# Optimization experiments

Measured on AMD Instinct MI355X. Metric: run time of the kernel, lower is better.

## Reference

```python
import jax, jax.numpy as jnp
import numpy as np

N = 100000   # nodes per graph
E = 1200000  # edges per graph
V = 50000    # vocab
EMB = 100    # embedding size
H = 64       # hidden size
B = 4096     # selected nodes (batch)
TIMESTEPS = 3  # per layer, layer_timesteps=[3,3]


def setup_inputs() -> dict:
    key = jax.random.key(0)
    ks = jax.random.split(key, 32)
    s = 0.05
    d = {}
    d['emb_ind_0'] = jax.random.randint(ks[0], (N,), 0, V)
    d['emb_ind_1'] = jax.random.randint(ks[1], (N,), 0, V)
    d['adj_0'] = jax.random.randint(ks[2], (E, 2), 0, N)
    d['adj_1'] = jax.random.randint(ks[3], (E, 2), 0, N)
    d['prop_ind_0'] = jax.random.randint(ks[4], (B,), 0, N)
    d['prop_ind_1'] = jax.random.randint(ks[5], (B,), 0, N)
    d['labels'] = jax.random.randint(ks[6], (B,), 0, 2)
    # embedding table (padding_idx=0 row zeroed)
    emb = jax.random.normal(ks[7], (V, EMB), jnp.float32) * s
    d['emb_table'] = emb.at[0].set(0.0)
    # emb_proj Linear(EMB, H)
    d['Wp'] = jax.random.normal(ks[8], (EMB, H), jnp.float32) * s
    d['bp'] = jnp.zeros((H,), jnp.float32)
    # GGNN: 2 layers, 1 edge type each; edge message Linear + GRUCell
    for l in range(2):
        o = 9 + 6 * l
        d[f'Wm{l}'] = jax.random.normal(ks[o + 0], (H, H), jnp.float32) * s
        d[f'bm{l}'] = jnp.zeros((H,), jnp.float32)
        d[f'Wih{l}'] = jax.random.normal(ks[o + 2], (H, 3 * H), jnp.float32) * s
        d[f'Whh{l}'] = jax.random.normal(ks[o + 3], (H, 3 * H), jnp.float32) * s
        d[f'bih{l}'] = jnp.zeros((3 * H,), jnp.float32)
        d[f'bhh{l}'] = jnp.zeros((3 * H,), jnp.float32)
    # classifier MLP: Linear(2H, H) -> ReLU -> Linear(H, 1) (dropout = identity in eval)
    d['W1'] = jax.random.normal(ks[22], (2 * H, H), jnp.float32) * s
    d['b1'] = jnp.zeros((H,), jnp.float32)
    d['W2'] = jax.random.normal(ks[23], (H, 1), jnp.float32) * s
    d['b2'] = jnp.zeros((1,), jnp.float32)
    return d


def gru_cell(x, h, Wih, Whh, bih, bhh):
    gi = x @ Wih + bih                       # [N, 3H]
    gh = h @ Whh + bhh
    ir, iz, ig = jnp.split(gi, 3, axis=-1)   # torch GRUCell gate order: r, z, n
    hr, hz, hg = jnp.split(gh, 3, axis=-1)
    r = jax.nn.sigmoid(ir + hr)
    z = jax.nn.sigmoid(iz + hz)
    n = jnp.tanh(ig + r * hg)
    return (1.0 - z) * n + z * h


def ggnn(h, edges, layer_params):
    src, tgt = edges[:, 0], edges[:, 1]
    n_nodes = h.shape[0]
    for (Wm, bm, Wih, Whh, bih, bhh) in layer_params:
        for _ in range(TIMESTEPS):
            msg = h[src] @ Wm + bm                                  # gather + edge transform [E, H]
            agg = jax.ops.segment_sum(msg, tgt, num_segments=n_nodes)  # scatter-add [N, H]
            h = gru_cell(agg, h, Wih, Whh, bih, bhh)
    return h


def reference(emb_ind_0, emb_ind_1, adj_0, adj_1, prop_ind_0, prop_ind_1, labels,
              emb_table, Wp, bp,
              Wm0, bm0, Wih0, Whh0, bih0, bhh0,
              Wm1, bm1, Wih1, Whh1, bih1, bhh1,
              W1, b1, W2, b2):
    layer_params = [(Wm0, bm0, Wih0, Whh0, bih0, bhh0),
                    (Wm1, bm1, Wih1, Whh1, bih1, bhh1)]
    ge_list = []
    for emb_ind, adj, prop_ind in ((emb_ind_0, adj_0, prop_ind_0),
                                   (emb_ind_1, adj_1, prop_ind_1)):
        ge = emb_table[emb_ind] @ Wp + bp        # embed + project [N, H]
        ge = ggnn(ge, adj, layer_params)
        ge_list.append(ge[prop_ind])             # index_select [B, H]
    ge = jnp.concatenate(ge_list, axis=-1)       # [B, 2H]
    hidden = jax.nn.relu(ge @ W1 + b1)
    z = hidden @ W2 + b2                         # [B, 1]
    probs = jax.nn.sigmoid(z)                    # torch code returns sigmoid as 'logits'
    y = labels.astype(z.dtype)
    zf = z[:, 0]
    # BCELoss(sigmoid(z), y), stably: log p = log_sigmoid(z), log(1-p) = log_sigmoid(-z)
    loss = -jnp.mean(y * jax.nn.log_sigmoid(zf) + (1.0 - y) * jax.nn.log_sigmoid(-zf))
    return (probs, loss)
```

## Files before the change

### kernel.cpp

```cpp
#include <hip/hip_runtime.h>
#include <math.h>

#define NN 100000
#define NN2 200000
#define NE 1200000
#define EMBD 100
#define HD 64
#define BT 4096
#define SCAN_B 196

typedef __attribute__((ext_vector_type(8))) short short8;
typedef __attribute__((ext_vector_type(4))) float f32x4;
typedef __attribute__((ext_vector_type(2))) float f32x2;

__device__ __forceinline__ float sig1(float x) { return 1.f / (1.f + __expf(-x)); }
__device__ __forceinline__ float tanh1(float x) {
    x = fminf(fmaxf(x, -15.f), 15.f);
    float e = __expf(2.f * x);
    return (e - 1.f) / (e + 1.f);
}
__device__ __forceinline__ unsigned short f2b(float f) {
    unsigned u = __float_as_uint(f);
    u += 0x7fffu + ((u >> 16) & 1u);
    return (unsigned short)(u >> 16);
}
__device__ __forceinline__ unsigned short hi16(float f) {
    return (unsigned short)(__float_as_uint(f) >> 16);
}
__device__ __forceinline__ unsigned packb(float lo, float hi) {
    return (unsigned)f2b(lo) | ((unsigned)f2b(hi) << 16);
}
__device__ __forceinline__ unsigned pk8(float a, float b, float c, float d) {
    int w = 0;
    w = __builtin_amdgcn_cvt_pk_fp8_f32(a, b, w, false);
    w = __builtin_amdgcn_cvt_pk_fp8_f32(c, d, w, true);
    return (unsigned)w;
}
__device__ __forceinline__ short8 f8frag(uint2 u) {
    const f32x2 a0 = __builtin_amdgcn_cvt_pk_f32_fp8(u.x, false);
    const f32x2 a1 = __builtin_amdgcn_cvt_pk_f32_fp8(u.x, true);
    const f32x2 a2 = __builtin_amdgcn_cvt_pk_f32_fp8(u.y, false);
    const f32x2 a3 = __builtin_amdgcn_cvt_pk_f32_fp8(u.y, true);
    short8 r;
    r[0] = (short)hi16(a0.x); r[1] = (short)hi16(a0.y);
    r[2] = (short)hi16(a1.x); r[3] = (short)hi16(a1.y);
    r[4] = (short)hi16(a2.x); r[5] = (short)hi16(a2.y);
    r[6] = (short)hi16(a3.x); r[7] = (short)hi16(a3.y);
    return r;
}

__global__ __launch_bounds__(256) void fusew_kernel(
    const float* __restrict__ Wm0, const float* __restrict__ Wih0, const float* __restrict__ bm0,
    const float* __restrict__ Wm1, const float* __restrict__ Wih1, const float* __restrict__ bm1,
    float* __restrict__ Wf, float* __restrict__ bf) {
    extern __shared__ float lds[];
    float* wm_s = lds;
    float* wih_s = lds + 4096;
    const int l = blockIdx.x >> 3, slice = blockIdx.x & 7;
    const float* Wm = l ? Wm1 : Wm0;
    const float* Wih = l ? Wih1 : Wih0;
    const float* bm = l ? bm1 : bm0;
    for (int i = threadIdx.x; i < 4096; i += 256) wm_s[i] = Wm[i];
    for (int i = threadIdx.x; i < 12288; i += 256) wih_s[i] = Wih[i];
    __syncthreads();
    float* Wfl = Wf + l * 12288;
    float* bfl = bf + l * 192;
    const int o0 = slice * 1536;
    for (int o = o0 + threadIdx.x; o < o0 + 1536; o += 256) {
        int r = o / 192, c = o % 192;
        float s = 0.f;
        for (int k = 0; k < 64; ++k) s = fmaf(wm_s[r * 64 + k], wih_s[k * 192 + c], s);
        Wfl[o] = s;
    }
    const int c0 = slice * 24;
    for (int c = c0 + threadIdx.x; c < c0 + 24; c += 256) {
        float s = 0.f;
        for (int k = 0; k < 64; ++k) s = fmaf(bm[k], wih_s[k * 192 + c], s);
        bfl[c] = s;
    }
}

__global__ __launch_bounds__(64) void wpack_kernel(
    const float* __restrict__ Wf, const float* __restrict__ Whh0, const float* __restrict__ Whh1,
    unsigned short* __restrict__ Wpk) {
    const int b = blockIdx.x;
    const int l = b >> 6, frag = b & 63;
    const int nt = frag >> 2, kk = frag & 3;
    const int lane = threadIdx.x;
    const int n = nt * 16 + (lane & 15);
    const int g = n >> 6, j = n & 63;
    const int k0 = kk * 32 + (lane >> 4) * 8;
    const float* wf = Wf + l * 12288;
    const float* whh = l ? Whh1 : Whh0;
    unsigned short o[8];
#pragma unroll
    for (int jj = 0; jj < 8; ++jj) {
        const int k = k0 + jj;
        float v = 0.f;
        if (k < 64) {
            const int kp = (k & 3) * 16 + (k >> 2);
            if (g == 0) v = wf[kp * 192 + j];
            else if (g == 1) v = wf[kp * 192 + 64 + j];
            else if (g == 2) v = wf[kp * 192 + 128 + j];
        } else {
            const int kp = ((k - 64) & 3) * 16 + ((k - 64) >> 2);
            if (g == 0) v = whh[kp * 192 + j];
            else if (g == 1) v = whh[kp * 192 + 64 + j];
            else if (g == 3) v = whh[kp * 192 + 128 + j];
        }
        o[jj] = f2b(v);
    }
    *(uint4*)(Wpk + ((size_t)(l * 64 + frag) * 64 + lane) * 8) = *(const uint4*)o;
}

__global__ __launch_bounds__(256) void embed_kernel(
    const int* __restrict__ ind0, const int* __restrict__ ind1, const float* __restrict__ emb,
    const float* __restrict__ Wp, const float* __restrict__ bp,
    unsigned char* __restrict__ hb8) {
    __shared__ float et[4][EMBD][4];
    const int w = threadIdx.x >> 6;
    const int l = threadIdx.x & 63;
    const int nodeBase = blockIdx.x * 16 + w * 4;
    for (int f = l; f < 100; f += 64) {
        const int n = f / 25, c = f % 25;
        const int gn = nodeBase + n;
        const int idx = (gn < NN) ? ind0[gn] : ind1[gn - NN];
        const float4 v = *(const float4*)(emb + (size_t)idx * EMBD + c * 4);
        et[w][c * 4 + 0][n] = v.x;
        et[w][c * 4 + 1][n] = v.y;
        et[w][c * 4 + 2][n] = v.z;
        et[w][c * 4 + 3][n] = v.w;
    }
    __syncthreads();
    float acc[4];
    acc[0] = bp[l]; acc[1] = acc[0]; acc[2] = acc[0]; acc[3] = acc[0];
#pragma unroll 5
    for (int k = 0; k < EMBD; ++k) {
        const float wv = Wp[k * 64 + l];
        const float4 ev = *(const float4*)&et[w][k][0];
        acc[0] = fmaf(ev.x, wv, acc[0]);
        acc[1] = fmaf(ev.y, wv, acc[1]);
        acc[2] = fmaf(ev.z, wv, acc[2]);
        acc[3] = fmaf(ev.w, wv, acc[3]);
    }
#pragma unroll
    for (int n = 0; n < 4; ++n) {
        const float v0 = __shfl(acc[n], l & 15);
        const float v1 = __shfl(acc[n], (l & 15) + 16);
        const float v2 = __shfl(acc[n], (l & 15) + 32);
        const float v3 = __shfl(acc[n], (l & 15) + 48);
        if (l < 16) ((unsigned*)(hb8 + (size_t)(nodeBase + n) * 64))[l] = pk8(v0, v1, v2, v3);
    }
}

__global__ __launch_bounds__(256) void hist_kernel(
    const int* __restrict__ adj0, const int* __restrict__ adj1, int* __restrict__ rowptr,
    int* __restrict__ rank) {
    const int e = blockIdx.x * 256 + threadIdx.x;
    const int tgt = (e < NE) ? adj0[2 * e + 1] : adj1[2 * (e - NE) + 1] + NN;
    rank[e] = atomicAdd(&rowptr[tgt], 1);
}

__global__ __launch_bounds__(256) void scan1_kernel(const int* __restrict__ rowptr, int* __restrict__ bsum) {
    __shared__ int red[256];
    const int t = threadIdx.x, b = blockIdx.x;
    const int base = b * 1024;
    int s = 0;
    for (int i = t; i < 1024; i += 256) {
        const int idx = base + i;
        s += (idx < NN2) ? rowptr[idx] : 0;
    }
    red[t] = s;
    __syncthreads();
    for (int off = 128; off > 0; off >>= 1) {
        if (t < off) red[t] += red[t + off];
        __syncthreads();
    }
    if (t == 0) bsum[b] = red[0];
}

__global__ __launch_bounds__(256) void scan2_kernel(int* __restrict__ bsum) {
    __shared__ int s[256];
    const int t = threadIdx.x;
    const int v = (t < SCAN_B) ? bsum[t] : 0;
    s[t] = v;
    __syncthreads();
    for (int off = 1; off < 256; off <<= 1) {
        const int x = (t >= off) ? s[t - off] : 0;
        __syncthreads();
        s[t] += x;
        __syncthreads();
    }
    if (t < SCAN_B) bsum[t] = s[t] - v;
}

__global__ __launch_bounds__(256) void scan3_kernel(int* __restrict__ rowptr, const int* __restrict__ bsum,
                                                    float* __restrict__ deg) {
    __shared__ int red[256];
    const int t = threadIdx.x, b = blockIdx.x;
    const int i0 = b * 1024 + t * 4;
    int v[4];
#pragma unroll
    for (int j = 0; j < 4; ++j) v[j] = (i0 + j < NN2) ? rowptr[i0 + j] : 0;
    const int ts = v[0] + v[1] + v[2] + v[3];
    red[t] = ts;
    __syncthreads();
    for (int off = 1; off < 256; off <<= 1) {
        const int x = (t >= off) ? red[t - off] : 0;
        __syncthreads();
        red[t] += x;
        __syncthreads();
    }
    int pre = bsum[b] + red[t] - ts;
#pragma unroll
    for (int j = 0; j < 4; ++j) {
        if (i0 + j < NN2) {
            rowptr[i0 + j] = pre;
            deg[i0 + j] = (float)v[j];
            pre += v[j];
        }
    }
}

__global__ __launch_bounds__(256) void fill_kernel(
    const int* __restrict__ adj0, const int* __restrict__ adj1,
    const int* __restrict__ rowptr, const int* __restrict__ rank, int* __restrict__ csr) {
    const int e = blockIdx.x * 256 + threadIdx.x;
    int2 st;
    int off;
    if (e < NE) {
        st = ((const int2*)adj0)[e];
        off = 0;
    } else {
        st = ((const int2*)adj1)[e - NE];
        off = NN;
    }
    const int tgt = st.y + off;
    csr[rowptr[tgt] + rank[e]] = st.x + off;
}

__global__ __launch_bounds__(256) void agg_kernel(
    const int* __restrict__ rowptr, const int* __restrict__ csr,
    const unsigned char* __restrict__ hb8, unsigned short* __restrict__ aggb) {
    const int t = threadIdx.x;
    const int node = blockIdx.x * 64 + (t >> 2);
    const int c = t & 3;
    const int start = rowptr[node];
    const int end = (node + 1 < NN2) ? rowptr[node + 1] : 2 * NE;
    float acc[16];
#pragma unroll
    for (int j = 0; j < 16; ++j) acc[j] = 0.f;
    int e = start;
    for (; e + 3 < end; e += 4) {
        int s[4];
        uint4 u[4];
#pragma unroll
        for (int q = 0; q < 4; ++q) s[q] = csr[e + q];
#pragma unroll
        for (int q = 0; q < 4; ++q) u[q] = *(const uint4*)(hb8 + (size_t)s[q] * 64 + c * 16);
#pragma unroll
        for (int q = 0; q < 4; ++q) {
            const f32x2 a0 = __builtin_amdgcn_cvt_pk_f32_fp8(u[q].x, false);
            const f32x2 a1 = __builtin_amdgcn_cvt_pk_f32_fp8(u[q].x, true);
            const f32x2 a2 = __builtin_amdgcn_cvt_pk_f32_fp8(u[q].y, false);
            const f32x2 a3 = __builtin_amdgcn_cvt_pk_f32_fp8(u[q].y, true);
            const f32x2 a4 = __builtin_amdgcn_cvt_pk_f32_fp8(u[q].z, false);
            const f32x2 a5 = __builtin_amdgcn_cvt_pk_f32_fp8(u[q].z, true);
            const f32x2 a6 = __builtin_amdgcn_cvt_pk_f32_fp8(u[q].w, false);
            const f32x2 a7 = __builtin_amdgcn_cvt_pk_f32_fp8(u[q].w, true);
            acc[0] += a0.x; acc[1] += a0.y; acc[2] += a1.x; acc[3] += a1.y;
            acc[4] += a2.x; acc[5] += a2.y; acc[6] += a3.x; acc[7] += a3.y;
            acc[8] += a4.x; acc[9] += a4.y; acc[10] += a5.x; acc[11] += a5.y;
            acc[12] += a6.x; acc[13] += a6.y; acc[14] += a7.x; acc[15] += a7.y;
        }
    }
    for (; e < end; ++e) {
        const uint4 u = *(const uint4*)(hb8 + (size_t)csr[e] * 64 + c * 16);
        const f32x2 a0 = __builtin_amdgcn_cvt_pk_f32_fp8(u.x, false);
        const f32x2 a1 = __builtin_amdgcn_cvt_pk_f32_fp8(u.x, true);
        const f32x2 a2 = __builtin_amdgcn_cvt_pk_f32_fp8(u.y, false);
        const f32x2 a3 = __builtin_amdgcn_cvt_pk_f32_fp8(u.y, true);
        const f32x2 a4 = __builtin_amdgcn_cvt_pk_f32_fp8(u.z, false);
        const f32x2 a5 = __builtin_amdgcn_cvt_pk_f32_fp8(u.z, true);
        const f32x2 a6 = __builtin_amdgcn_cvt_pk_f32_fp8(u.w, false);
        const f32x2 a7 = __builtin_amdgcn_cvt_pk_f32_fp8(u.w, true);
        acc[0] += a0.x; acc[1] += a0.y; acc[2] += a1.x; acc[3] += a1.y;
        acc[4] += a2.x; acc[5] += a2.y; acc[6] += a3.x; acc[7] += a3.y;
        acc[8] += a4.x; acc[9] += a4.y; acc[10] += a5.x; acc[11] += a5.y;
        acc[12] += a6.x; acc[13] += a6.y; acc[14] += a7.x; acc[15] += a7.y;
    }
    uint4 o0, o1;
    o0.x = packb(acc[0], acc[1]);
    o0.y = packb(acc[2], acc[3]);
    o0.z = packb(acc[4], acc[5]);
    o0.w = packb(acc[6], acc[7]);
    o1.x = packb(acc[8], acc[9]);
    o1.y = packb(acc[10], acc[11]);
    o1.z = packb(acc[12], acc[13]);
    o1.w = packb(acc[14], acc[15]);
    *(uint4*)(aggb + node * 64 + c * 16) = o0;
    *(uint4*)(aggb + node * 64 + c * 16 + 8) = o1;
}

__global__ __launch_bounds__(256) void aggx_kernel(
    const int* __restrict__ prop0, const int* __restrict__ prop1,
    const int* __restrict__ rowptr, const int* __restrict__ csr,
    const unsigned char* __restrict__ hb8, unsigned short* __restrict__ aggX) {
    const int t = threadIdx.x;
    const int p = blockIdx.x * 64 + (t >> 2);
    const int c = t & 3;
    const int node = (p < BT) ? prop0[p] : NN + prop1[p - BT];
    const int start = rowptr[node];
    const int end = (node + 1 < NN2) ? rowptr[node + 1] : 2 * NE;
    float acc[16];
#pragma unroll
    for (int j = 0; j < 16; ++j) acc[j] = 0.f;
    for (int e = start; e < end; ++e) {
        const uint4 u = *(const uint4*)(hb8 + (size_t)csr[e] * 64 + c * 16);
        const f32x2 a0 = __builtin_amdgcn_cvt_pk_f32_fp8(u.x, false);
        const f32x2 a1 = __builtin_amdgcn_cvt_pk_f32_fp8(u.x, true);
        const f32x2 a2 = __builtin_amdgcn_cvt_pk_f32_fp8(u.y, false);
        const f32x2 a3 = __builtin_amdgcn_cvt_pk_f32_fp8(u.y, true);
        const f32x2 a4 = __builtin_amdgcn_cvt_pk_f32_fp8(u.z, false);
        const f32x2 a5 = __builtin_amdgcn_cvt_pk_f32_fp8(u.z, true);
        const f32x2 a6 = __builtin_amdgcn_cvt_pk_f32_fp8(u.w, false);
        const f32x2 a7 = __builtin_amdgcn_cvt_pk_f32_fp8(u.w, true);
        acc[0] += a0.x; acc[1] += a0.y; acc[2] += a1.x; acc[3] += a1.y;
        acc[4] += a2.x; acc[5] += a2.y; acc[6] += a3.x; acc[7] += a3.y;
        acc[8] += a4.x; acc[9] += a4.y; acc[10] += a5.x; acc[11] += a5.y;
        acc[12] += a6.x; acc[13] += a6.y; acc[14] += a7.x; acc[15] += a7.y;
    }
    uint4 o0, o1;
    o0.x = packb(acc[0], acc[1]);
    o0.y = packb(acc[2], acc[3]);
    o0.z = packb(acc[4], acc[5]);
    o0.w = packb(acc[6], acc[7]);
    o1.x = packb(acc[8], acc[9]);
    o1.y = packb(acc[10], acc[11]);
    o1.z = packb(acc[12], acc[13]);
    o1.w = packb(acc[14], acc[15]);
    *(uint4*)(aggX + p * 64 + c * 16) = o0;
    *(uint4*)(aggX + p * 64 + c * 16 + 8) = o1;
}

__global__ __launch_bounds__(256) void gru_mfma_kernel(
    unsigned char* __restrict__ hb8, const unsigned short* __restrict__ aggb,
    const float* __restrict__ deg, const unsigned short* __restrict__ Wpk,
    const float* __restrict__ bf, const float* __restrict__ bih, const float* __restrict__ bhh) {
    extern __shared__ unsigned short ldsW[];
    {
        const uint4* src = (const uint4*)Wpk;
        uint4* dst = (uint4*)ldsW;
        for (int i = threadIdx.x; i < 4096; i += 256) dst[i] = src[i];
    }
    __syncthreads();
    const int lane = threadIdx.x & 63;
    const int j0 = lane & 15, quad = lane >> 4;
    const int q8 = quad * 8;
    float cr[4], cz[4], cig[4], chg[4], vbfr[4], vbfz[4], vbfg[4];
#pragma unroll
    for (int c4 = 0; c4 < 4; ++c4) {
        const int col = c4 * 16 + j0;
        cr[c4] = bih[col] + bhh[col];
        cz[c4] = bih[64 + col] + bhh[64 + col];
        cig[c4] = bih[128 + col];
        chg[c4] = bhh[128 + col];
        vbfr[c4] = bf[col];
        vbfz[c4] = bf[64 + col];
        vbfg[c4] = bf[128 + col];
    }
    const short8* ldsW8 = (const short8*)ldsW;
    const int gw = blockIdx.x * 4 + (threadIdx.x >> 6);
    const int nw = gridDim.x * 4;

    auto epilogue = [&](const f32x4(&acc)[16], int nb) {
#pragma unroll
        for (int reg = 0; reg < 4; ++reg) {
            const int node = nb + reg;
            const float dg = deg[node];
            const unsigned hu = *(const unsigned*)(hb8 + (size_t)node * 64 + j0 * 4);
            const f32x2 h01 = __builtin_amdgcn_cvt_pk_f32_fp8(hu, false);
            const f32x2 h23 = __builtin_amdgcn_cvt_pk_f32_fp8(hu, true);
            const float holdf[4] = {h01.x, h01.y, h23.x, h23.y};
            float hn[4];
#pragma unroll
            for (int c4 = 0; c4 < 4; ++c4) {
                const float rv = sig1(acc[c4][reg] + cr[c4] + dg * vbfr[c4]);
                const float zv = sig1(acc[4 + c4][reg] + cz[c4] + dg * vbfz[c4]);
                const float gi = acc[8 + c4][reg] + cig[c4] + dg * vbfg[c4];
                const float gh = acc[12 + c4][reg] + chg[c4];
                const float nv = tanh1(fmaf(rv, gh, gi));
                hn[c4] = (1.f - zv) * nv + zv * holdf[c4];
            }
            ((unsigned*)(hb8 + (size_t)node * 64))[j0] = pk8(hn[0], hn[1], hn[2], hn[3]);
        }
    };

    for (int t = gw; t < NN2 / 32; t += nw) {
        const int mbase = t * 32;
        const int node0 = mbase + j0, node1 = node0 + 16;
        short8 a[4], b[4];
        a[0] = *(const short8*)(aggb + node0 * 64 + q8);
        a[1] = *(const short8*)(aggb + node0 * 64 + 32 + q8);
        a[2] = f8frag(*(const uint2*)(hb8 + (size_t)node0 * 64 + q8));
        a[3] = f8frag(*(const uint2*)(hb8 + (size_t)node0 * 64 + 32 + q8));
        b[0] = *(const short8*)(aggb + node1 * 64 + q8);
        b[1] = *(const short8*)(aggb + node1 * 64 + 32 + q8);
        b[2] = f8frag(*(const uint2*)(hb8 + (size_t)node1 * 64 + q8));
        b[3] = f8frag(*(const uint2*)(hb8 + (size_t)node1 * 64 + 32 + q8));
        f32x4 acc0[16], acc1[16];
#pragma unroll
        for (int i = 0; i < 16; ++i) {
            acc0[i] = (f32x4){0.f, 0.f, 0.f, 0.f};
            acc1[i] = (f32x4){0.f, 0.f, 0.f, 0.f};
        }
#pragma unroll
        for (int nt = 0; nt < 16; ++nt) {
#pragma unroll
            for (int kk = 0; kk < 4; ++kk) {
                const short8 w = ldsW8[(nt * 4 + kk) * 64 + lane];
                acc0[nt] = __builtin_amdgcn_mfma_f32_16x16x32_bf16(a[kk], w, acc0[nt], 0, 0, 0);
                acc1[nt] = __builtin_amdgcn_mfma_f32_16x16x32_bf16(b[kk], w, acc1[nt], 0, 0, 0);
            }
        }
        epilogue(acc0, mbase + quad * 4);
        epilogue(acc1, mbase + 16 + quad * 4);
    }
}

__global__ __launch_bounds__(256) void grux_kernel(
    const int* __restrict__ prop0, const int* __restrict__ prop1,
    const unsigned char* __restrict__ hb8, const unsigned short* __restrict__ aggX,
    const float* __restrict__ deg, const unsigned short* __restrict__ Wpk,
    const float* __restrict__ bf, const float* __restrict__ bih, const float* __restrict__ bhh,
    float* __restrict__ X) {
    extern __shared__ unsigned short ldsW[];
    {
        const uint4* src = (const uint4*)Wpk;
        uint4* dst = (uint4*)ldsW;
        for (int i = threadIdx.x; i < 4096; i += 256) dst[i] = src[i];
    }
    __syncthreads();
    const int lane = threadIdx.x & 63;
    const int j0 = lane & 15, quad = lane >> 4;
    const int q8 = quad * 8;
    float cr[4], cz[4], cig[4], chg[4], vbfr[4], vbfz[4], vbfg[4];
#pragma unroll
    for (int c4 = 0; c4 < 4; ++c4) {
        const int col = c4 * 16 + j0;
        cr[c4] = bih[col] + bhh[col];
        cz[c4] = bih[64 + col] + bhh[64 + col];
        cig[c4] = bih[128 + col];
        chg[c4] = bhh[128 + col];
        vbfr[c4] = bf[col];
        vbfz[c4] = bf[64 + col];
        vbfg[c4] = bf[128 + col];
    }
    const short8* ldsW8 = (const short8*)ldsW;
    const int gw = blockIdx.x * 4 + (threadIdx.x >> 6);

    auto mapnode = [&](int p) { return (p < BT) ? prop0[p] : NN + prop1[p - BT]; };

    auto epilogue = [&](const f32x4(&acc)[16], int pb) {
#pragma unroll
        for (int reg = 0; reg < 4; ++reg) {
            const int p = pb + reg;
            const int node = mapnode(p);
            const float dg = deg[node];
            const unsigned hu = *(const unsigned*)(hb8 + (size_t)node * 64 + j0 * 4);
            const f32x2 h01 = __builtin_amdgcn_cvt_pk_f32_fp8(hu, false);
            const f32x2 h23 = __builtin_amdgcn_cvt_pk_f32_fp8(hu, true);
            const float holdf[4] = {h01.x, h01.y, h23.x, h23.y};
            const int b = p & (BT - 1), g = p >> 12;
            float* xr = X + b * 128 + g * 64;
#pragma unroll
            for (int c4 = 0; c4 < 4; ++c4) {
                const int col = c4 * 16 + j0;
                const float rv = sig1(acc[c4][reg] + cr[c4] + dg * vbfr[c4]);
                const float zv = sig1(acc[4 + c4][reg] + cz[c4] + dg * vbfz[c4]);
                const float gi = acc[8 + c4][reg] + cig[c4] + dg * vbfg[c4];
                const float gh = acc[12 + c4][reg] + chg[c4];
                const float nv = tanh1(fmaf(rv, gh, gi));
                xr[col] = (1.f - zv) * nv + zv * holdf[c4];
            }
        }
    };

    const int mbase = gw * 32;
    const int p0 = mbase + j0, p1 = p0 + 16;
    const int node0 = mapnode(p0), node1 = mapnode(p1);
    short8 a[4], b[4];
    a[0] = *(const short8*)(aggX + p0 * 64 + q8);
    a[1] = *(const short8*)(aggX + p0 * 64 + 32 + q8);
    a[2] = f8frag(*(const uint2*)(hb8 + (size_t)node0 * 64 + q8));
    a[3] = f8frag(*(const uint2*)(hb8 + (size_t)node0 * 64 + 32 + q8));
    b[0] = *(const short8*)(aggX + p1 * 64 + q8);
    b[1] = *(const short8*)(aggX + p1 * 64 + 32 + q8);
    b[2] = f8frag(*(const uint2*)(hb8 + (size_t)node1 * 64 + q8));
    b[3] = f8frag(*(const uint2*)(hb8 + (size_t)node1 * 64 + 32 + q8));
    f32x4 acc0[16], acc1[16];
#pragma unroll
    for (int i = 0; i < 16; ++i) {
        acc0[i] = (f32x4){0.f, 0.f, 0.f, 0.f};
        acc1[i] = (f32x4){0.f, 0.f, 0.f, 0.f};
    }
#pragma unroll
    for (int nt = 0; nt < 16; ++nt) {
#pragma unroll
        for (int kk = 0; kk < 4; ++kk) {
            const short8 w = ldsW8[(nt * 4 + kk) * 64 + lane];
            acc0[nt] = __builtin_amdgcn_mfma_f32_16x16x32_bf16(a[kk], w, acc0[nt], 0, 0, 0);
            acc1[nt] = __builtin_amdgcn_mfma_f32_16x16x32_bf16(b[kk], w, acc1[nt], 0, 0, 0);
        }
    }
    epilogue(acc0, mbase + quad * 4);
    epilogue(acc1, mbase + 16 + quad * 4);
}

__global__ __launch_bounds__(256) void mlp_kernel(
    const float* __restrict__ X, const float* __restrict__ W1, const float* __restrict__ b1,
    const float* __restrict__ W2, const float* __restrict__ b2,
    float* __restrict__ out, float* __restrict__ zbuf) {
    const int b = blockIdx.x * 4 + (threadIdx.x >> 6);
    const int j = threadIdx.x & 63;
    const float* x = X + b * 128;
    float acc = b1[j];
#pragma unroll 4
    for (int k = 0; k < 128; ++k) acc = fmaf(x[k], W1[k * 64 + j], acc);
    float v = fmaxf(acc, 0.f) * W2[j];
#pragma unroll
    for (int off = 32; off > 0; off >>= 1) v += __shfl_down(v, off);
    if (j == 0) {
        const float z = v + b2[0];
        out[b] = 1.f / (1.f + expf(-z));
        zbuf[b] = z;
    }
}

__global__ __launch_bounds__(256) void loss_kernel(
    const float* __restrict__ zbuf, const int* __restrict__ labels, float* __restrict__ out) {
    __shared__ float red[256];
    const int t = threadIdx.x;
    float s = 0.f;
    for (int i = t; i < BT; i += 256) {
        const float z = zbuf[i];
        const float y = (float)labels[i];
        const float lsp = (z >= 0.f) ? -log1pf(expf(-z)) : (z - log1pf(expf(z)));
        const float lsn = lsp - z;
        s += y * lsp + (1.f - y) * lsn;
    }
    red[t] = s;
    __syncthreads();
    for (int off = 128; off > 0; off >>= 1) {
        if (t < off) red[t] += red[t + off];
        __syncthreads();
    }
    if (t == 0) out[BT] = -red[0] / (float)BT;
}

extern "C" void kernel_launch(void* const* d_in, const int* in_sizes, int n_in,
                              void* d_out, int out_size, void* d_ws, size_t ws_size,
                              hipStream_t stream) {
    char* ws = (char*)d_ws;
    unsigned short* aggb = (unsigned short*)(ws);
    unsigned char* hb8 = (unsigned char*)(ws + 25600000);
    float* deg = (float*)(ws + 38400000);
    float* Wf = (float*)(ws + 39200000);
    float* bf = (float*)(ws + 39298304);
    int* rowptr = (int*)(ws + 39299840);
    int* csr = (int*)(ws + 40099840);
    int* bsum = (int*)(ws + 49699840);
    unsigned short* Wpk = (unsigned short*)(ws + 49700864);
    unsigned short* aggX = (unsigned short*)(ws + 49831936);
    int* rank = (int*)(ws);
    float* X = (float*)(ws);
    float* zbuf = (float*)(ws + 2097152);
    float* out = (float*)d_out;

    const float* emb_table = (const float*)d_in[7];
    const float* Wp = (const float*)d_in[8];
    const float* bp = (const float*)d_in[9];
    const int* prop0 = (const int*)d_in[4];
    const int* prop1 = (const int*)d_in[5];

    fusew_kernel<<<16, 256, 65536, stream>>>(
        (const float*)d_in[10], (const float*)d_in[12], (const float*)d_in[11],
        (const float*)d_in[16], (const float*)d_in[18], (const float*)d_in[17], Wf, bf);
    wpack_kernel<<<128, 64, 0, stream>>>(Wf, (const float*)d_in[13], (const float*)d_in[19], Wpk);

    hipMemsetAsync(rowptr, 0, (size_t)NN2 * 4, stream);
    hist_kernel<<<2 * NE / 256, 256, 0, stream>>>((const int*)d_in[2], (const int*)d_in[3], rowptr,
                                                  rank);
    scan1_kernel<<<SCAN_B, 256, 0, stream>>>(rowptr, bsum);
    scan2_kernel<<<1, 256, 0, stream>>>(bsum);
    scan3_kernel<<<SCAN_B, 256, 0, stream>>>(rowptr, bsum, deg);
    fill_kernel<<<2 * NE / 256, 256, 0, stream>>>((const int*)d_in[2], (const int*)d_in[3], rowptr,
                                                  rank, csr);

    embed_kernel<<<NN2 / 16, 256, 0, stream>>>((const int*)d_in[0], (const int*)d_in[1], emb_table,
                                               Wp, bp, hb8);

    for (int l = 0; l < 2; ++l) {
        const float* bih = (const float*)d_in[14 + 6 * l];
        const float* bhh = (const float*)d_in[15 + 6 * l];
        for (int ts = 0; ts < 3; ++ts) {
            if (l == 1 && ts == 2) {
                aggx_kernel<<<2 * BT / 64, 256, 0, stream>>>(prop0, prop1, rowptr, csr, hb8, aggX);
                grux_kernel<<<64, 256, 65536, stream>>>(prop0, prop1, hb8, aggX, deg,
                                                        Wpk + l * 32768, bf + l * 192, bih, bhh, X);
            } else {
                agg_kernel<<<NN2 / 64, 256, 0, stream>>>(rowptr, csr, hb8, aggb);
                gru_mfma_kernel<<<512, 256, 65536, stream>>>(hb8, aggb, deg, Wpk + l * 32768,
                                                             bf + l * 192, bih, bhh);
            }
        }
    }

    mlp_kernel<<<BT / 4, 256, 0, stream>>>(X, (const float*)d_in[22], (const float*)d_in[23],
                                           (const float*)d_in[24], (const float*)d_in[25], out, zbuf);
    loss_kernel<<<1, 256, 0, stream>>>(zbuf, (const int*)d_in[6], out);
}
```

Baseline: 879.1 us.

## Fuse neighbor aggregation into GRU MFMA kernel with ping-pong hidden buffers

Merges the separate aggregation and GRU kernels into one kernel. Each block gathers neighbor sums for 128 nodes into swizzled LDS as bf16, then runs the MFMA GRU update straight from LDS. The bf16 aggregate no longer makes a round trip through global memory, and five launches are saved. Two fp8 hidden buffers are swapped between steps because a node's update now races with neighbors still reading its old state. In exchange, each block uses 80KB of LDS, which lowers occupancy for the gather-heavy phase, and each node's gather uses 2 threads instead of 4.

```diff
diff --git a/kernel.cpp b/kernel.cpp
--- a/kernel.cpp
+++ b/kernel.cpp
@@ -47,6 +47,20 @@
     r[4] = (short)hi16(a2.x); r[5] = (short)hi16(a2.y);
     r[6] = (short)hi16(a3.x); r[7] = (short)hi16(a3.y);
     return r;
+}
+__device__ __forceinline__ void acc16(float* acc, uint4 u) {
+    const f32x2 a0 = __builtin_amdgcn_cvt_pk_f32_fp8(u.x, false);
+    const f32x2 a1 = __builtin_amdgcn_cvt_pk_f32_fp8(u.x, true);
+    const f32x2 a2 = __builtin_amdgcn_cvt_pk_f32_fp8(u.y, false);
+    const f32x2 a3 = __builtin_amdgcn_cvt_pk_f32_fp8(u.y, true);
+    const f32x2 a4 = __builtin_amdgcn_cvt_pk_f32_fp8(u.z, false);
+    const f32x2 a5 = __builtin_amdgcn_cvt_pk_f32_fp8(u.z, true);
+    const f32x2 a6 = __builtin_amdgcn_cvt_pk_f32_fp8(u.w, false);
+    const f32x2 a7 = __builtin_amdgcn_cvt_pk_f32_fp8(u.w, true);
+    acc[0] += a0.x; acc[1] += a0.y; acc[2] += a1.x; acc[3] += a1.y;
+    acc[4] += a2.x; acc[5] += a2.y; acc[6] += a3.x; acc[7] += a3.y;
+    acc[8] += a4.x; acc[9] += a4.y; acc[10] += a5.x; acc[11] += a5.y;
+    acc[12] += a6.x; acc[13] += a6.y; acc[14] += a7.x; acc[15] += a7.y;
 }
 
 __global__ __launch_bounds__(256) void fusew_kernel(
@@ -239,67 +253,141 @@
     csr[rowptr[tgt] + rank[e]] = st.x + off;
 }
 
-__global__ __launch_bounds__(256) void agg_kernel(
+__global__ __launch_bounds__(256) void agru_kernel(
+    const unsigned char* __restrict__ hsrc, unsigned char* __restrict__ hdst,
     const int* __restrict__ rowptr, const int* __restrict__ csr,
-    const unsigned char* __restrict__ hb8, unsigned short* __restrict__ aggb) {
-    const int t = threadIdx.x;
-    const int node = blockIdx.x * 64 + (t >> 2);
-    const int c = t & 3;
-    const int start = rowptr[node];
-    const int end = (node + 1 < NN2) ? rowptr[node + 1] : 2 * NE;
-    float acc[16];
-#pragma unroll
-    for (int j = 0; j < 16; ++j) acc[j] = 0.f;
-    int e = start;
-    for (; e + 3 < end; e += 4) {
-        int s[4];
-        uint4 u[4];
-#pragma unroll
-        for (int q = 0; q < 4; ++q) s[q] = csr[e + q];
-#pragma unroll
-        for (int q = 0; q < 4; ++q) u[q] = *(const uint4*)(hb8 + (size_t)s[q] * 64 + c * 16);
-#pragma unroll
-        for (int q = 0; q < 4; ++q) {
-            const f32x2 a0 = __builtin_amdgcn_cvt_pk_f32_fp8(u[q].x, false);
-            const f32x2 a1 = __builtin_amdgcn_cvt_pk_f32_fp8(u[q].x, true);
-            const f32x2 a2 = __builtin_amdgcn_cvt_pk_f32_fp8(u[q].y, false);
-            const f32x2 a3 = __builtin_amdgcn_cvt_pk_f32_fp8(u[q].y, true);
-            const f32x2 a4 = __builtin_amdgcn_cvt_pk_f32_fp8(u[q].z, false);
-            const f32x2 a5 = __builtin_amdgcn_cvt_pk_f32_fp8(u[q].z, true);
-            const f32x2 a6 = __builtin_amdgcn_cvt_pk_f32_fp8(u[q].w, false);
-            const f32x2 a7 = __builtin_amdgcn_cvt_pk_f32_fp8(u[q].w, true);
-            acc[0] += a0.x; acc[1] += a0.y; acc[2] += a1.x; acc[3] += a1.y;
-            acc[4] += a2.x; acc[5] += a2.y; acc[6] += a3.x; acc[7] += a3.y;
-            acc[8] += a4.x; acc[9] += a4.y; acc[10] += a5.x; acc[11] += a5.y;
-            acc[12] += a6.x; acc[13] += a6.y; acc[14] += a7.x; acc[15] += a7.y;
+    const float* __restrict__ deg, const unsigned short* __restrict__ Wpk,
+    const float* __restrict__ bf, const float* __restrict__ bih, const float* __restrict__ bhh) {
+    extern __shared__ unsigned short ldsag[];
+    unsigned short* ldsW = ldsag;
+    char* ldsA = (char*)(ldsag + 32768);
+    {
+        const uint4* src = (const uint4*)Wpk;
+        uint4* dst = (uint4*)ldsW;
+        for (int i = threadIdx.x; i < 4096; i += 256) dst[i] = src[i];
+    }
+    const int tid = threadIdx.x;
+
+    {
+        const int nl = tid >> 1;
+        const int c2 = tid & 1;
+        const int node = blockIdx.x * 128 + nl;
+        if (node < NN2) {
+            const int start = rowptr[node];
+            const int end = (node + 1 < NN2) ? rowptr[node + 1] : 2 * NE;
+            float acc[32];
+#pragma unroll
+            for (int j = 0; j < 32; ++j) acc[j] = 0.f;
+            int e = start;
+            for (; e + 1 < end; e += 2) {
+                const int s0 = csr[e], s1 = csr[e + 1];
+                const uint4 u0 = *(const uint4*)(hsrc + (size_t)s0 * 64 + c2 * 32);
+                const uint4 u1 = *(const uint4*)(hsrc + (size_t)s0 * 64 + c2 * 32 + 16);
+                const uint4 v0 = *(const uint4*)(hsrc + (size_t)s1 * 64 + c2 * 32);
+                const uint4 v1 = *(const uint4*)(hsrc + (size_t)s1 * 64 + c2 * 32 + 16);
+                acc16(acc, u0);
+                acc16(acc + 16, u1);
+                acc16(acc, v0);
+                acc16(acc + 16, v1);
+            }
+            if (e < end) {
+                const int s0 = csr[e];
+                const uint4 u0 = *(const uint4*)(hsrc + (size_t)s0 * 64 + c2 * 32);
+                const uint4 u1 = *(const uint4*)(hsrc + (size_t)s0 * 64 + c2 * 32 + 16);
+                acc16(acc, u0);
+                acc16(acc + 16, u1);
+            }
+            const int rowb = nl * 128 + c2 * 64;
+#pragma unroll
+            for (int k = 0; k < 4; ++k) {
+                uint4 o;
+                o.x = packb(acc[k * 8 + 0], acc[k * 8 + 1]);
+                o.y = packb(acc[k * 8 + 2], acc[k * 8 + 3]);
+                o.z = packb(acc[k * 8 + 4], acc[k * 8 + 5]);
+                o.w = packb(acc[k * 8 + 6], acc[k * 8 + 7]);
+                const int byteoff = (rowb + k * 16) ^ ((nl & 7) << 4);
+                *(uint4*)(ldsA + byteoff) = o;
+            }
         }
     }
-    for (; e < end; ++e) {
-        const uint4 u = *(const uint4*)(hb8 + (size_t)csr[e] * 64 + c * 16);
-        const f32x2 a0 = __builtin_amdgcn_cvt_pk_f32_fp8(u.x, false);
-        const f32x2 a1 = __builtin_amdgcn_cvt_pk_f32_fp8(u.x, true);
-        const f32x2 a2 = __builtin_amdgcn_cvt_pk_f32_fp8(u.y, false);
-        const f32x2 a3 = __builtin_amdgcn_cvt_pk_f32_fp8(u.y, true);
-        const f32x2 a4 = __builtin_amdgcn_cvt_pk_f32_fp8(u.z, false);
-        const f32x2 a5 = __builtin_amdgcn_cvt_pk_f32_fp8(u.z, true);
-        const f32x2 a6 = __builtin_amdgcn_cvt_pk_f32_fp8(u.w, false);
-        const f32x2 a7 = __builtin_amdgcn_cvt_pk_f32_fp8(u.w, true);
-        acc[0] += a0.x; acc[1] += a0.y; acc[2] += a1.x; acc[3] += a1.y;
-        acc[4] += a2.x; acc[5] += a2.y; acc[6] += a3.x; acc[7] += a3.y;
-        acc[8] += a4.x; acc[9] += a4.y; acc[10] += a5.x; acc[11] += a5.y;
-        acc[12] += a6.x; acc[13] += a6.y; acc[14] += a7.x; acc[15] += a7.y;
-    }
-    uint4 o0, o1;
-    o0.x = packb(acc[0], acc[1]);
-    o0.y = packb(acc[2], acc[3]);
-    o0.z = packb(acc[4], acc[5]);
-    o0.w = packb(acc[6], acc[7]);
-    o1.x = packb(acc[8], acc[9]);
-    o1.y = packb(acc[10], acc[11]);
-    o1.z = packb(acc[12], acc[13]);
-    o1.w = packb(acc[14], acc[15]);
-    *(uint4*)(aggb + node * 64 + c * 16) = o0;
-    *(uint4*)(aggb + node * 64 + c * 16 + 8) = o1;
+    __syncthreads();
+
+    const int lane = tid & 63;
+    const int w = tid >> 6;
+    const int j0 = lane & 15, quad = lane >> 4;
+    const int q8 = quad * 8;
+    const int mbase = blockIdx.x * 128 + w * 32;
+    if (mbase >= NN2) return;
+
+    float cr[4], cz[4], cig[4], chg[4], vbfr[4], vbfz[4], vbfg[4];
+#pragma unroll
+    for (int c4 = 0; c4 < 4; ++c4) {
+        const int col = c4 * 16 + j0;
+        cr[c4] = bih[col] + bhh[col];
+        cz[c4] = bih[64 + col] + bhh[64 + col];
+        cig[c4] = bih[128 + col];
+        chg[c4] = bhh[128 + col];
+        vbfr[c4] = bf[col];
+        vbfz[c4] = bf[64 + col];
+        vbfg[c4] = bf[128 + col];
+    }
+    const short8* ldsW8 = (const short8*)ldsW;
+    auto ldA = [&](int r, int half) -> short8 {
+        const int byteoff = (r * 128 + half * 64 + quad * 16) ^ ((r & 7) << 4);
+        return *(const short8*)(ldsA + byteoff);
+    };
+
+    const int r0 = w * 32 + j0, r1 = r0 + 16;
+    const int node0 = mbase + j0, node1 = node0 + 16;
+    short8 a[4], b[4];
+    a[0] = ldA(r0, 0);
+    a[1] = ldA(r0, 1);
+    a[2] = f8frag(*(const uint2*)(hsrc + (size_t)node0 * 64 + q8));
+    a[3] = f8frag(*(const uint2*)(hsrc + (size_t)node0 * 64 + 32 + q8));
+    b[0] = ldA(r1, 0);
+    b[1] = ldA(r1, 1);
+    b[2] = f8frag(*(const uint2*)(hsrc + (size_t)node1 * 64 + q8));
+    b[3] = f8frag(*(const uint2*)(hsrc + (size_t)node1 * 64 + 32 + q8));
+    f32x4 acc0[16], acc1[16];
+#pragma unroll
+    for (int i = 0; i < 16; ++i) {
+        acc0[i] = (f32x4){0.f, 0.f, 0.f, 0.f};
+        acc1[i] = (f32x4){0.f, 0.f, 0.f, 0.f};
+    }
+#pragma unroll
+    for (int nt = 0; nt < 16; ++nt) {
+#pragma unroll
+        for (int kk = 0; kk < 4; ++kk) {
+            const short8 wv = ldsW8[(nt * 4 + kk) * 64 + lane];
+            acc0[nt] = __builtin_amdgcn_mfma_f32_16x16x32_bf16(a[kk], wv, acc0[nt], 0, 0, 0);
+            acc1[nt] = __builtin_amdgcn_mfma_f32_16x16x32_bf16(b[kk], wv, acc1[nt], 0, 0, 0);
+        }
+    }
+
+    auto epilogue = [&](const f32x4(&acc)[16], int nb) {
+#pragma unroll
+        for (int reg = 0; reg < 4; ++reg) {
+            const int node = nb + reg;
+            const float dg = deg[node];
+            const unsigned hu = *(const unsigned*)(hsrc + (size_t)node * 64 + j0 * 4);
+            const f32x2 h01 = __builtin_amdgcn_cvt_pk_f32_fp8(hu, false);
+            const f32x2 h23 = __builtin_amdgcn_cvt_pk_f32_fp8(hu, true);
+            const float holdf[4] = {h01.x, h01.y, h23.x, h23.y};
+            float hn[4];
+#pragma unroll
+            for (int c4 = 0; c4 < 4; ++c4) {
+                const float rv = sig1(acc[c4][reg] + cr[c4] + dg * vbfr[c4]);
+                const float zv = sig1(acc[4 + c4][reg] + cz[c4] + dg * vbfz[c4]);
+                const float gi = acc[8 + c4][reg] + cig[c4] + dg * vbfg[c4];
+                const float gh = acc[12 + c4][reg] + chg[c4];
+                const float nv = tanh1(fmaf(rv, gh, gi));
+                hn[c4] = (1.f - zv) * nv + zv * holdf[c4];
+            }
+            ((unsigned*)(hdst + (size_t)node * 64))[j0] = pk8(hn[0], hn[1], hn[2], hn[3]);
+        }
+    };
+    epilogue(acc0, mbase + quad * 4);
+    epilogue(acc1, mbase + 16 + quad * 4);
 }
 
 __global__ __launch_bounds__(256) void aggx_kernel(
@@ -317,18 +405,7 @@
     for (int j = 0; j < 16; ++j) acc[j] = 0.f;
     for (int e = start; e < end; ++e) {
         const uint4 u = *(const uint4*)(hb8 + (size_t)csr[e] * 64 + c * 16);
-        const f32x2 a0 = __builtin_amdgcn_cvt_pk_f32_fp8(u.x, false);
-        const f32x2 a1 = __builtin_amdgcn_cvt_pk_f32_fp8(u.x, true);
-        const f32x2 a2 = __builtin_amdgcn_cvt_pk_f32_fp8(u.y, false);
-        const f32x2 a3 = __builtin_amdgcn_cvt_pk_f32_fp8(u.y, true);
-        const f32x2 a4 = __builtin_amdgcn_cvt_pk_f32_fp8(u.z, false);
-        const f32x2 a5 = __builtin_amdgcn_cvt_pk_f32_fp8(u.z, true);
-        const f32x2 a6 = __builtin_amdgcn_cvt_pk_f32_fp8(u.w, false);
-        const f32x2 a7 = __builtin_amdgcn_cvt_pk_f32_fp8(u.w, true);
-        acc[0] += a0.x; acc[1] += a0.y; acc[2] += a1.x; acc[3] += a1.y;
-        acc[4] += a2.x; acc[5] += a2.y; acc[6] += a3.x; acc[7] += a3.y;
-        acc[8] += a4.x; acc[9] += a4.y; acc[10] += a5.x; acc[11] += a5.y;
-        acc[12] += a6.x; acc[13] += a6.y; acc[14] += a7.x; acc[15] += a7.y;
+        acc16(acc, u);
     }
     uint4 o0, o1;
     o0.x = packb(acc[0], acc[1]);
@@ -341,91 +418,6 @@
     o1.w = packb(acc[14], acc[15]);
     *(uint4*)(aggX + p * 64 + c * 16) = o0;
     *(uint4*)(aggX + p * 64 + c * 16 + 8) = o1;
-}
-
-__global__ __launch_bounds__(256) void gru_mfma_kernel(
-    unsigned char* __restrict__ hb8, const unsigned short* __restrict__ aggb,
-    const float* __restrict__ deg, const unsigned short* __restrict__ Wpk,
-    const float* __restrict__ bf, const float* __restrict__ bih, const float* __restrict__ bhh) {
-    extern __shared__ unsigned short ldsW[];
-    {
-        const uint4* src = (const uint4*)Wpk;
-        uint4* dst = (uint4*)ldsW;
-        for (int i = threadIdx.x; i < 4096; i += 256) dst[i] = src[i];
-    }
-    __syncthreads();
-    const int lane = threadIdx.x & 63;
-    const int j0 = lane & 15, quad = lane >> 4;
-    const int q8 = quad * 8;
-    float cr[4], cz[4], cig[4], chg[4], vbfr[4], vbfz[4], vbfg[4];
-#pragma unroll
-    for (int c4 = 0; c4 < 4; ++c4) {
-        const int col = c4 * 16 + j0;
-        cr[c4] = bih[col] + bhh[col];
-        cz[c4] = bih[64 + col] + bhh[64 + col];
-        cig[c4] = bih[128 + col];
-        chg[c4] = bhh[128 + col];
-        vbfr[c4] = bf[col];
-        vbfz[c4] = bf[64 + col];
-        vbfg[c4] = bf[128 + col];
-    }
-    const short8* ldsW8 = (const short8*)ldsW;
-    const int gw = blockIdx.x * 4 + (threadIdx.x >> 6);
-    const int nw = gridDim.x * 4;
-
-    auto epilogue = [&](const f32x4(&acc)[16], int nb) {
-#pragma unroll
-        for (int reg = 0; reg < 4; ++reg) {
-            const int node = nb + reg;
-            const float dg = deg[node];
-            const unsigned hu = *(const unsigned*)(hb8 + (size_t)node * 64 + j0 * 4);
-            const f32x2 h01 = __builtin_amdgcn_cvt_pk_f32_fp8(hu, false);
-            const f32x2 h23 = __builtin_amdgcn_cvt_pk_f32_fp8(hu, true);
-            const float holdf[4] = {h01.x, h01.y, h23.x, h23.y};
-            float hn[4];
-#pragma unroll
-            for (int c4 = 0; c4 < 4; ++c4) {
-                const float rv = sig1(acc[c4][reg] + cr[c4] + dg * vbfr[c4]);
-                const float zv = sig1(acc[4 + c4][reg] + cz[c4] + dg * vbfz[c4]);
-                const float gi = acc[8 + c4][reg] + cig[c4] + dg * vbfg[c4];
-                const float gh = acc[12 + c4][reg] + chg[c4];
-                const float nv = tanh1(fmaf(rv, gh, gi));
-                hn[c4] = (1.f - zv) * nv + zv * holdf[c4];
-            }
-            ((unsigned*)(hb8 + (size_t)node * 64))[j0] = pk8(hn[0], hn[1], hn[2], hn[3]);
-        }
-    };
-
-    for (int t = gw; t < NN2 / 32; t += nw) {
-        const int mbase = t * 32;
-        const int node0 = mbase + j0, node1 = node0 + 16;
-        short8 a[4], b[4];
-        a[0] = *(const short8*)(aggb + node0 * 64 + q8);
-        a[1] = *(const short8*)(aggb + node0 * 64 + 32 + q8);
-        a[2] = f8frag(*(const uint2*)(hb8 + (size_t)node0 * 64 + q8));
-        a[3] = f8frag(*(const uint2*)(hb8 + (size_t)node0 * 64 + 32 + q8));
-        b[0] = *(const short8*)(aggb + node1 * 64 + q8);
-        b[1] = *(const short8*)(aggb + node1 * 64 + 32 + q8);
-        b[2] = f8frag(*(const uint2*)(hb8 + (size_t)node1 * 64 + q8));
-        b[3] = f8frag(*(const uint2*)(hb8 + (size_t)node1 * 64 + 32 + q8));
-        f32x4 acc0[16], acc1[16];
-#pragma unroll
-        for (int i = 0; i < 16; ++i) {
-            acc0[i] = (f32x4){0.f, 0.f, 0.f, 0.f};
-            acc1[i] = (f32x4){0.f, 0.f, 0.f, 0.f};
-        }
-#pragma unroll
-        for (int nt = 0; nt < 16; ++nt) {
-#pragma unroll
-            for (int kk = 0; kk < 4; ++kk) {
-                const short8 w = ldsW8[(nt * 4 + kk) * 64 + lane];
-                acc0[nt] = __builtin_amdgcn_mfma_f32_16x16x32_bf16(a[kk], w, acc0[nt], 0, 0, 0);
-                acc1[nt] = __builtin_amdgcn_mfma_f32_16x16x32_bf16(b[kk], w, acc1[nt], 0, 0, 0);
-            }
-        }
-        epilogue(acc0, mbase + quad * 4);
-        epilogue(acc1, mbase + 16 + quad * 4);
-    }
 }
 
 __global__ __launch_bounds__(256) void grux_kernel(
@@ -562,8 +554,8 @@
                               void* d_out, int out_size, void* d_ws, size_t ws_size,
                               hipStream_t stream) {
     char* ws = (char*)d_ws;
-    unsigned short* aggb = (unsigned short*)(ws);
-    unsigned char* hb8 = (unsigned char*)(ws + 25600000);
+    unsigned char* hb8B = (unsigned char*)(ws);
+    unsigned char* hb8A = (unsigned char*)(ws + 25600000);
     float* deg = (float*)(ws + 38400000);
     float* Wf = (float*)(ws + 39200000);
     float* bf = (float*)(ws + 39298304);
@@ -598,22 +590,24 @@
                                                   rank, csr);
 
     embed_kernel<<<NN2 / 16, 256, 0, stream>>>((const int*)d_in[0], (const int*)d_in[1], emb_table,
-                                               Wp, bp, hb8);
-
-    for (int l = 0; l < 2; ++l) {
+                                               Wp, bp, hb8B);
+
+    for (int s = 0; s < 5; ++s) {
+        const int l = (s < 3) ? 0 : 1;
+        const unsigned char* src = (s & 1) ? hb8A : hb8B;
+        unsigned char* dst = (s & 1) ? hb8B : hb8A;
         const float* bih = (const float*)d_in[14 + 6 * l];
         const float* bhh = (const float*)d_in[15 + 6 * l];
-        for (int ts = 0; ts < 3; ++ts) {
-            if (l == 1 && ts == 2) {
-                aggx_kernel<<<2 * BT / 64, 256, 0, stream>>>(prop0, prop1, rowptr, csr, hb8, aggX);
-                grux_kernel<<<64, 256, 65536, stream>>>(prop0, prop1, hb8, aggX, deg,
-                                                        Wpk + l * 32768, bf + l * 192, bih, bhh, X);
-            } else {
-                agg_kernel<<<NN2 / 64, 256, 0, stream>>>(rowptr, csr, hb8, aggb);
-                gru_mfma_kernel<<<512, 256, 65536, stream>>>(hb8, aggb, deg, Wpk + l * 32768,
-                                                             bf + l * 192, bih, bhh);
-            }
-        }
+        agru_kernel<<<(NN2 + 127) / 128, 256, 81920, stream>>>(
+            src, dst, rowptr, csr, deg, Wpk + l * 32768, bf + l * 192, bih, bhh);
+    }
+
+    {
+        const float* bih = (const float*)d_in[20];
+        const float* bhh = (const float*)d_in[21];
+        aggx_kernel<<<2 * BT / 64, 256, 0, stream>>>(prop0, prop1, rowptr, csr, hb8A, aggX);
+        grux_kernel<<<64, 256, 65536, stream>>>(prop0, prop1, hb8A, aggX, deg, Wpk + 32768,
+                                                bf + 192, bih, bhh, X);
     }
 
     mlp_kernel<<<BT / 4, 256, 0, stream>>>(X, (const float*)d_in[22], (const float*)d_in[23],
```

Result: slower. 1.081 ms (+22.9%).
